# Optimization experiments

Measured on AMD Instinct MI355X. Metric: run time of the kernel, lower is better.

The kernel has to match this reference:

```python
import jax, jax.numpy as jnp
import numpy as np

B, T, V, D, E, A, F = 128, 20, 10000, 1024, 1024, 1024, 2048
ARNET_W = 0.005


def setup_inputs() -> dict:
    key = jax.random.key(0)
    ks = jax.random.split(key, 32)
    p = lambda i, shape: jax.random.normal(ks[i], shape, jnp.float32) * 0.02
    sizes = jax.random.randint(ks[2], (B - 1, 1), 3, T + 1)
    sizes = jnp.concatenate([jnp.array([[T]], dtype=sizes.dtype), sizes], axis=0)  # force max = T
    return dict(
        feats=jax.random.normal(ks[0], (B, 36, F), jnp.float32),
        sequences=jax.random.randint(ks[1], (B, T), 0, V),
        sizes=sizes,
        emb=p(3, (V, E)),
        td_wi=p(4, (4 * D, E + F + D)), td_wh=p(5, (4 * D, D)), td_bi=p(6, (4 * D,)), td_bh=p(7, (4 * D,)),
        lg_wi=p(8, (4 * D, F + D)), lg_wh=p(9, (4 * D, D)), lg_bi=p(10, (4 * D,)), lg_bh=p(11, (4 * D,)),
        ar_wi=p(12, (4 * D, D)), ar_wh=p(13, (4 * D, D)), ar_bi=p(14, (4 * D,)), ar_bh=p(15, (4 * D,)),
        arl_w=p(16, (D, D)), arl_b=p(17, (D,)),
        out_w=p(18, (V, D)), out_b=p(19, (V,)),
        af_w=p(20, (A, F)), af_b=p(21, (A,)),
        ad_w=p(22, (A, D)), ad_b=p(23, (A,)),
        aw_w=p(24, (1, A)), aw_b=p(25, (1,)),
    )


def _lstm(x, h, c, wi, wh, bi, bh):
    # torch.nn.LSTMCell: gates ordered i, f, g, o
    g = x @ wi.T + bi + h @ wh.T + bh
    i, f, gg, o = jnp.split(g, 4, axis=1)
    c2 = jax.nn.sigmoid(f) * c + jax.nn.sigmoid(i) * jnp.tanh(gg)
    return jax.nn.sigmoid(o) * jnp.tanh(c2), c2


def reference(feats, sequences, sizes, emb,
              td_wi, td_wh, td_bi, td_bh,
              lg_wi, lg_wh, lg_bi, lg_bh,
              ar_wi, ar_wh, ar_bi, ar_bh,
              arl_w, arl_b, out_w, out_b,
              af_w, af_b, ad_w, ad_b, aw_w, aw_b):
    # Sort by caption length descending (torch.sort descending)
    order = jnp.argsort(-sizes[:, 0])
    sizes_s = sizes[order, 0]
    feats = feats[order]
    seqs = sequences[order]
    dec_len = sizes_s - 1                      # decode_lengths, max == T-1 by construction
    Tdec = seqs.shape[1] - 1
    featsAvg = feats.mean(axis=1)              # [B, F]
    embs = emb[seqs]                           # [B, T, E]
    # Attention image projection is timestep-invariant: precompute
    img_att = jnp.einsum('brf,af->bra', feats, af_w) + af_b  # [B, 36, A]
    zeros = jnp.zeros((B, D), feats.dtype)

    def step(carry, xs):
        h1, c1, h2, c2, arh, arc, prev_h1, loss = carry
        t, emb_t = xs
        m = (dec_len > t)[:, None].astype(feats.dtype)   # [B,1] active mask (== torch [:bSize] slice)
        bs = m.sum()
        # Top-down LSTM
        nh1, nc1 = _lstm(jnp.concatenate([h2, featsAvg, emb_t], axis=1), h1, c1, td_wi, td_wh, td_bi, td_bh)
        h1 = m * nh1 + (1.0 - m) * h1
        c1 = m * nc1 + (1.0 - m) * c1
        # Visual attention over 36 regions (dropout is identity in eval)
        h1a = h1 @ ad_w.T + ad_b                         # [B, A]
        e = jnp.maximum(h1a[:, None, :] + img_att, 0.0) @ aw_w[0] + aw_b[0]  # [B, 36]
        alpha = jax.nn.softmax(e, axis=1)
        awe = jnp.einsum('br,brf->bf', alpha, feats)     # [B, F]
        # Language LSTM
        nh2, nc2 = _lstm(jnp.concatenate([awe, h1], axis=1), h2, c2, lg_wi, lg_wh, lg_bi, lg_bh)
        h2 = m * nh2 + (1.0 - m) * h2
        c2 = m * nc2 + (1.0 - m) * c2
        # ARNet reconstruction LSTM
        narh, narc = _lstm(h1, arh, arc, ar_wi, ar_wh, ar_bi, ar_bh)
        arh = m * narh + (1.0 - m) * arh
        arc = m * narc + (1.0 - m) * arc
        diff = (arh @ arl_w.T + arl_b) - prev_h1
        lt = jnp.sum(m[:, 0] * jnp.sum(diff * diff, axis=1)) / bs * ARNET_W
        loss = loss + jnp.where(t > 0, lt, jnp.zeros((), feats.dtype))
        pred = m * (h2 @ out_w.T + out_b)                # [B, V], zeros for finished rows
        return (h1, c1, h2, c2, arh, arc, h1, loss), pred

    init = (zeros, zeros, zeros, zeros, zeros, zeros, zeros, jnp.zeros((), feats.dtype))
    xs = (jnp.arange(Tdec), jnp.swapaxes(embs[:, :Tdec], 0, 1))
    (_, _, _, _, _, _, _, loss_ar), preds = jax.lax.scan(step, init, xs)
    preds = jnp.swapaxes(preds, 0, 1)                    # [B, Tdec, V]
    return preds, seqs, order, loss_ar
```

## Files before the change

kernel.cpp:

```cpp
#include <hip/hip_runtime.h>
#include <math.h>

#define B    128
#define T    20
#define TD   19
#define V    10000
#define D    1024
#define E    1024
#define A_DIM 1024
#define F    2048
#define NR   36
#define BD   (B * D)

typedef __attribute__((ext_vector_type(8))) short bf16x8;
typedef __attribute__((ext_vector_type(4))) float f32x4;

__device__ __forceinline__ float sigm(float x) { return 1.f / (1.f + __expf(-x)); }

__device__ __forceinline__ unsigned short f2bf(float f) {
    union { float f; unsigned u; } x; x.f = f;
    unsigned r = x.u + 0x7fffu + ((x.u >> 16) & 1u);
    return (unsigned short)(r >> 16);
}
__device__ __forceinline__ float bf2f(unsigned short u) {
    union { float f; unsigned u; } x; x.u = ((unsigned)u) << 16; return x.f;
}
__device__ __forceinline__ uint4 pack8(const float* __restrict__ src) {
    float4 a = *(const float4*)src, b = *(const float4*)(src + 4);
    union { unsigned short u[8]; uint4 v; } p;
    p.u[0] = f2bf(a.x); p.u[1] = f2bf(a.y); p.u[2] = f2bf(a.z); p.u[3] = f2bf(a.w);
    p.u[4] = f2bf(b.x); p.u[5] = f2bf(b.y); p.u[6] = f2bf(b.z); p.u[7] = f2bf(b.w);
    return p.v;
}

__global__ void k_sort_init(const int* __restrict__ sizes,
                            const int* __restrict__ sequences,
                            int* __restrict__ order,
                            int* __restrict__ active,
                            int* __restrict__ seqs_s,
                            float* __restrict__ out)
{
    int tid = threadIdx.x;
    __shared__ int s_sizes[B];
    __shared__ int s_dl[B];
    s_sizes[tid] = sizes[tid];
    __syncthreads();
    int si = s_sizes[tid];
    int rank = 0;
    for (int j = 0; j < B; ++j) {
        int sj = s_sizes[j];
        if (sj > si || (sj == si && j < tid)) rank++;
    }
    order[rank] = tid;
    __syncthreads();
    int ob = order[tid];
    int dl = s_sizes[ob] - 1;
    s_dl[tid] = dl;
    for (int tt = 0; tt < T; ++tt) {
        int sq = sequences[ob * T + tt];
        seqs_s[tid * T + tt] = sq;
        out[(size_t)B * TD * V + tid * T + tt] = (float)sq;
    }
    out[(size_t)B * TD * V + B * T + tid] = (float)ob;
    __syncthreads();
    if (tid < TD) {
        int c = 0;
        for (int b = 0; b < B; ++b) c += (s_dl[b] > tid) ? 1 : 0;
        active[tid] = c;
    }
    if (tid == 0) out[(size_t)B * TD * V + B * T + B] = 0.f;
}

__global__ void k_zero(float* __restrict__ p, int n) {
    int i = blockIdx.x * 256 + threadIdx.x;
    if (i < n) p[i] = 0.f;
}

__global__ void k_w2bf(const float* __restrict__ s1, int K1,
                       const float* __restrict__ s2, int K2,
                       unsigned short* __restrict__ dst, long total ,
                       int il)
{
    long g = (long)blockIdx.x * 256 + threadIdx.x;
    if (g >= total) return;
    int Kt = K1 + K2;
    int gpr = Kt >> 3;
    int row = (int)(g / gpr);
    int k8 = (int)(g % gpr) << 3;
    if (k8 >= K1 && !s2) {
        uint4 z{};
        *(uint4*)(dst + ((size_t)g << 3)) = z;
        return;
    }
    int srow = il ? ((row & 3) * 1024 + (row >> 2)) : row;
    const float* src = (k8 < K1) ? (s1 + (size_t)srow * K1 + k8)
                                 : (s2 + (size_t)srow * K2 + (k8 - K1));
    *(uint4*)(dst + ((size_t)g << 3)) = pack8(src);
}

__global__ void k_feats2bf(const float* __restrict__ feats, const int* __restrict__ order,
                           unsigned short* __restrict__ dst)
{
    long g = (long)blockIdx.x * 256 + threadIdx.x;
    int row = (int)(g >> 8);
    int k8 = ((int)g & 255) << 3;
    int b = row / NR, r = row - b * NR;
    const float* src = feats + ((size_t)order[b] * NR + r) * F + k8;
    *(uint4*)(dst + (size_t)row * F + k8) = pack8(src);
}

__global__ void k_favg(const float* __restrict__ feats, const int* __restrict__ order,
                       unsigned short* __restrict__ xtd)
{
    int idx = blockIdx.x * 256 + threadIdx.x;
    int b = idx >> 11, f = idx & 2047;
    const float* base = feats + (size_t)order[b] * NR * F + f;
    float s = 0.f;
#pragma unroll
    for (int r = 0; r < NR; ++r) s += base[(size_t)r * F];
    xtd[(size_t)b * 5120 + 1024 + f] = f2bf(s * (1.f / NR));
}

__global__ void k_emb2bf(const float* __restrict__ emb, const int* __restrict__ seqs_s,
                         unsigned short* __restrict__ embs_bf)
{
    long g = (long)blockIdx.x * 256 + threadIdx.x;
    if (g >= (long)B * TD * 128) return;
    int b = (int)(g / (TD * 128));
    int rem = (int)(g - (long)b * (TD * 128));
    int t = rem >> 7, e8 = (rem & 127) << 3;
    const float* src = emb + (size_t)seqs_s[b * T + t] * E + e8;
    *(uint4*)(embs_bf + (((size_t)(b * TD + t)) << 10) + e8) = pack8(src);
}

__global__ void k_embslot(const unsigned short* __restrict__ embs_bf,
                          unsigned short* __restrict__ xtd, int t)
{
    int g = blockIdx.x * 256 + threadIdx.x;
    int b = g >> 7, e8 = (g & 127) << 3;
    *(uint4*)(xtd + (size_t)b * 5120 + 3072 + e8) =
        *(const uint4*)(embs_bf + (((size_t)(b * TD + t)) << 10) + e8);
}

__global__ void k_biasint(const float* __restrict__ bi, const float* __restrict__ bh,
                          const float* __restrict__ extra, float* __restrict__ dst, int n)
{
    int i = blockIdx.x * 256 + threadIdx.x;
    if (i >= n) return;
    if (i < 4096) {
        int j = i >> 2, g = i & 3;
        dst[i] = bi[g * 1024 + j] + bh[g * 1024 + j];
    } else {
        dst[i] = extra[i - 4096];
    }
}

__device__ __forceinline__ void gemm_core(
    const unsigned short* __restrict__ A, int lda,
    const unsigned short* __restrict__ W, int ldw, int Ksub, int N,
    unsigned short* __restrict__ smem,
    int bm, int bn, f32x4 (&acc)[2][2])
{
    int tid = threadIdx.x, l = tid & 63, w = tid >> 6;
    int rsel = l & 15, ksel = (l >> 4) * 8;

    const unsigned short* ap[4];
#pragma unroll
    for (int i = 0; i < 4; ++i) {
        int s = 4 * w + i, mt = s >> 1, subk = s & 1;
        ap[i] = A + (size_t)(bm + mt * 16 + rsel) * lda + subk * 32 + ksel;
    }
    int nt_w = w >> 1, wsub = w & 1;
    int nr = bn + nt_w * 16 + rsel; if (nr >= N) nr = N - 1;
    const unsigned short* wp = W + (size_t)nr * ldw + wsub * 32 + ksel;
    int ntile = Ksub >> 6;

    uint4 rA0_0, rA0_1, rA0_2, rA0_3, rW0;
    uint4 rA1_0, rA1_1, rA1_2, rA1_3, rW1;

    auto load0 = [&]() {
        rA0_0 = *(const uint4*)ap[0]; ap[0] += 64;
        rA0_1 = *(const uint4*)ap[1]; ap[1] += 64;
        rA0_2 = *(const uint4*)ap[2]; ap[2] += 64;
        rA0_3 = *(const uint4*)ap[3]; ap[3] += 64;
        rW0 = *(const uint4*)wp; wp += 64;
    };
    auto load1 = [&]() {
        rA1_0 = *(const uint4*)ap[0]; ap[0] += 64;
        rA1_1 = *(const uint4*)ap[1]; ap[1] += 64;
        rA1_2 = *(const uint4*)ap[2]; ap[2] += 64;
        rA1_3 = *(const uint4*)ap[3]; ap[3] += 64;
        rW1 = *(const uint4*)wp; wp += 64;
    };
    auto stash0 = [&]() {
        unsigned short* As = smem;
        *(uint4*)(As + (4 * w + 0) * 512 + l * 8) = rA0_0;
        *(uint4*)(As + (4 * w + 1) * 512 + l * 8) = rA0_1;
        *(uint4*)(As + (4 * w + 2) * 512 + l * 8) = rA0_2;
        *(uint4*)(As + (4 * w + 3) * 512 + l * 8) = rA0_3;
        *(uint4*)(As + 8192 + w * 512 + l * 8) = rW0;
    };
    auto stash1 = [&]() {
        unsigned short* As = smem + 10240;
        *(uint4*)(As + (4 * w + 0) * 512 + l * 8) = rA1_0;
        *(uint4*)(As + (4 * w + 1) * 512 + l * 8) = rA1_1;
        *(uint4*)(As + (4 * w + 2) * 512 + l * 8) = rA1_2;
        *(uint4*)(As + (4 * w + 3) * 512 + l * 8) = rA1_3;
        *(uint4*)(As + 8192 + w * 512 + l * 8) = rW1;
    };
    auto compute = [&](int p) {
        unsigned short* As = smem + p * 10240;
        unsigned short* Ws = As + 8192;
#pragma unroll
        for (int subk = 0; subk < 2; ++subk) {
            bf16x8 a0 = *(const bf16x8*)(As + (4 * w + subk) * 512 + l * 8);
            bf16x8 a1 = *(const bf16x8*)(As + (4 * w + 2 + subk) * 512 + l * 8);
            bf16x8 b0 = *(const bf16x8*)(Ws + subk * 512 + l * 8);
            bf16x8 b1 = *(const bf16x8*)(Ws + (2 + subk) * 512 + l * 8);
            acc[0][0] = __builtin_amdgcn_mfma_f32_16x16x32_bf16(a0, b0, acc[0][0], 0, 0, 0);
            acc[0][1] = __builtin_amdgcn_mfma_f32_16x16x32_bf16(a0, b1, acc[0][1], 0, 0, 0);
            acc[1][0] = __builtin_amdgcn_mfma_f32_16x16x32_bf16(a1, b0, acc[1][0], 0, 0, 0);
            acc[1][1] = __builtin_amdgcn_mfma_f32_16x16x32_bf16(a1, b1, acc[1][1], 0, 0, 0);
        }
    };

    load0(); load1();
    for (int t = 0; t < ntile; t += 2) {
        stash0();
        if (t + 2 < ntile) load0();
        asm volatile("s_waitcnt lgkmcnt(0)" ::: "memory");
        __builtin_amdgcn_s_barrier();
        compute(0);
        __builtin_amdgcn_s_barrier();
        stash1();
        if (t + 3 < ntile) load1();
        asm volatile("s_waitcnt lgkmcnt(0)" ::: "memory");
        __builtin_amdgcn_s_barrier();
        compute(1);
        __builtin_amdgcn_s_barrier();
    }
}

__global__ __launch_bounds__(256)
void k_gemm(const unsigned short* __restrict__ A, int lda,
            const unsigned short* __restrict__ W, int ldw, int Ksub,
            const float* __restrict__ bias,
            float* __restrict__ C, int ldc, int N,
            int mode, const float* __restrict__ sub, const int* __restrict__ actp,
            float* __restrict__ lossp)
{
    __shared__ __align__(16) unsigned short smem[2 * 10240];
    __shared__ float ps[4];

    int bn = blockIdx.x * 32, bm;
    const unsigned short* Ab = A;
    const unsigned short* Wb = W;
    float* Cb = C;
    if (mode == 4) {
        bm = 0;
        Ab += (size_t)blockIdx.y * Ksub;
        Wb += (size_t)blockIdx.y * Ksub;
        Cb  = C + (size_t)blockIdx.y * 128 * ldc;
    } else {
        bm = blockIdx.y * 128;
    }
    int tid = threadIdx.x, l = tid & 63, w = tid >> 6;

    f32x4 acc[2][2] = {};
    gemm_core(Ab, lda, Wb, ldw, Ksub, N, smem, bm, bn, acc);

    int rg4 = (l >> 4) * 4, cc = l & 15;
    if (mode == 1) {
        int act = actp[blockIdx.y];
        float s = 0.f;
#pragma unroll
        for (int mi = 0; mi < 2; ++mi) {
            int mt = 2 * w + mi;
#pragma unroll
            for (int ni = 0; ni < 2; ++ni) {
                int col = bn + ni * 16 + cc;
                float bb = bias[col];
#pragma unroll
                for (int rg = 0; rg < 4; ++rg) {
                    int row = bm + mt * 16 + rg4 + rg;
                    float v = acc[mi][ni][rg] + bb - sub[(size_t)row * 1024 + col];
                    if ((row & 127) < act) s += v * v;
                }
            }
        }
        for (int o = 32; o > 0; o >>= 1) s += __shfl_down(s, o, 64);
        if (l == 0) ps[w] = s;
        __syncthreads();
        if (tid == 0) {
            float tot = ps[0] + ps[1] + ps[2] + ps[3];
            atomicAdd(lossp, tot * (0.005f / (float)act));
        }
        return;
    }

    if (mode == 3) {
#pragma unroll
        for (int mi = 0; mi < 2; ++mi) {
            int mt = 2 * w + mi;
#pragma unroll
            for (int ni = 0; ni < 2; ++ni) {
                int col = bn + ni * 16 + cc;
                if (col >= N) continue;
                float bb = bias[col];
#pragma unroll
                for (int rg = 0; rg < 4; ++rg) {
                    int row = bm + mt * 16 + rg4 + rg;
                    int tt = row >> 7, b = row & 127;
                    float v = acc[mi][ni][rg] + bb;
                    if (b >= actp[tt]) v = 0.f;
                    C[(size_t)b * ((size_t)TD * V) + (size_t)tt * V + col] = v;
                }
            }
        }
        return;
    }

    if (mode == 4) {
#pragma unroll
        for (int mi = 0; mi < 2; ++mi) {
            int mt = 2 * w + mi;
#pragma unroll
            for (int ni = 0; ni < 2; ++ni) {
                int col = bn + ni * 16 + cc;
#pragma unroll
                for (int rg = 0; rg < 4; ++rg) {
                    int row = mt * 16 + rg4 + rg;
                    Cb[(size_t)row * ldc + col] = acc[mi][ni][rg];
                }
            }
        }
        return;
    }

#pragma unroll
    for (int mi = 0; mi < 2; ++mi) {
        int mt = 2 * w + mi;
#pragma unroll
        for (int ni = 0; ni < 2; ++ni) {
            int col = bn + ni * 16 + cc;
            if (col >= N) continue;
            float bb = bias[col];
#pragma unroll
            for (int rg = 0; rg < 4; ++rg) {
                int row = bm + mt * 16 + rg4 + rg;
                C[(size_t)row * ldc + col] = acc[mi][ni][rg] + bb;
            }
        }
    }
}

__global__ void k_lstm4(const float* __restrict__ p, int ldp, int ns,
                        const float* __restrict__ biasI,
                        float* __restrict__ h, float* __restrict__ c,
                        const int* __restrict__ actp, float* __restrict__ prevh,
                        unsigned short* __restrict__ s1, int ld1,
                        unsigned short* __restrict__ s2, int ld2,
                        unsigned short* __restrict__ s3, int ld3,
                        const unsigned short* __restrict__ embs_bf,
                        unsigned short* __restrict__ xtd_emb, int tnext)
{
    int idx = blockIdx.x * 256 + threadIdx.x;
    if (embs_bf && idx < B * 128) {
        int be = idx >> 7, e8 = (idx & 127) << 3;
        *(uint4*)(xtd_emb + (size_t)be * 5120 + 3072 + e8) =
            *(const uint4*)(embs_bf + (((size_t)(be * TD + tnext)) << 10) + e8);
    }
    int b = idx >> 10;
    if (b >= *actp) return;
    int j = idx & 1023;
    const float* pb = p + (size_t)b * ldp + (j << 2);
    size_t spl = (size_t)128 * ldp;
    float4 g = *(const float4*)pb;
    for (int s = 1; s < ns; ++s) {
        float4 gs = *(const float4*)(pb + (size_t)s * spl);
        g.x += gs.x; g.y += gs.y; g.z += gs.z; g.w += gs.w;
    }
    float4 bb = *(const float4*)(biasI + (j << 2));
    float gi = g.x + bb.x, gf = g.y + bb.y, gg = g.z + bb.z, go = g.w + bb.w;
    size_t ix = (size_t)b * 1024 + j;
    if (prevh) prevh[ix] = h[ix];
    float c2v = sigm(gf) * c[ix] + sigm(gi) * tanhf(gg);
    c[ix] = c2v;
    float hv = sigm(go) * tanhf(c2v);
    h[ix] = hv;
    unsigned short hb = f2bf(hv);
    if (s1) s1[(size_t)b * ld1 + j] = hb;
    if (s2) s2[(size_t)b * ld2 + j] = hb;
    if (s3) s3[(size_t)b * ld3 + j] = hb;
}

__global__ __launch_bounds__(256)
void k_attn_ar(const float* __restrict__ pc, const float* __restrict__ bias_comb,
               const float* __restrict__ img_att,
               const float* __restrict__ aw_w, const float* __restrict__ aw_b,
               const unsigned short* __restrict__ feats_bf,
               unsigned short* __restrict__ xlg,
               float* __restrict__ arh, float* __restrict__ arc,
               const int* __restrict__ actp,
               unsigned short* __restrict__ xar_slot,
               unsigned short* __restrict__ Arout_t)
{
    int b = blockIdx.x;
    int tid = threadIdx.x;
    __shared__ float sh[A_DIM];
    __shared__ float se[NR];
    const float* p0 = pc + (size_t)b * 5120;
    const float* p1 = pc + (size_t)128 * 5120 + (size_t)b * 5120;
    for (int a = tid; a < A_DIM; a += 256)
        sh[a] = p0[4096 + a] + p1[4096 + a] + bias_comb[4096 + a];

    int act = *actp;
    if (b < act) {
#pragma unroll
        for (int u = 0; u < 4; ++u) {
            int j = (tid << 2) + u;
            float4 ga = *(const float4*)(p0 + (j << 2));
            float4 gb = *(const float4*)(p1 + (j << 2));
            float4 bb = *(const float4*)(bias_comb + (j << 2));
            float gi = ga.x + gb.x + bb.x, gf = ga.y + gb.y + bb.y;
            float gg = ga.z + gb.z + bb.z, go = ga.w + gb.w + bb.w;
            size_t ix = (size_t)b * 1024 + j;
            float c2v = sigm(gf) * arc[ix] + sigm(gi) * tanhf(gg);
            arc[ix] = c2v;
            float hv = sigm(go) * tanhf(c2v);
            arh[ix] = hv;
            unsigned short hb = f2bf(hv);
            xar_slot[(size_t)b * 2048 + j] = hb;
            if (Arout_t) Arout_t[(size_t)b * 1024 + j] = hb;
        }
    }
    __syncthreads();

    int wid = tid >> 6, lane = tid & 63;
    for (int r = wid; r < NR; r += 4) {
        const float* row = img_att + ((size_t)b * NR + r) * A_DIM;
        float s = 0.f;
        for (int a = lane; a < A_DIM; a += 64)
            s += fmaxf(sh[a] + row[a], 0.f) * aw_w[a];
        for (int off = 32; off > 0; off >>= 1) s += __shfl_down(s, off, 64);
        if (lane == 0) se[r] = s + aw_b[0];
    }
    __syncthreads();
    if (tid == 0) {
        float m = se[0];
        for (int r = 1; r < NR; ++r) m = fmaxf(m, se[r]);
        float ssum = 0.f;
        for (int r = 0; r < NR; ++r) { float ex = __expf(se[r] - m); se[r] = ex; ssum += ex; }
        float inv = 1.f / ssum;
        for (int r = 0; r < NR; ++r) se[r] *= inv;
    }
    __syncthreads();
    int f8 = tid << 3;
    const unsigned short* fb = feats_bf + (size_t)b * NR * F + f8;
    float s[8] = {};
    for (int r = 0; r < NR; ++r) {
        bf16x8 v = *(const bf16x8*)(fb + (size_t)r * F);
        float a = se[r];
#pragma unroll
        for (int q = 0; q < 8; ++q)
            s[q] += a * bf2f(((const unsigned short*)&v)[q]);
    }
    union { unsigned short u[8]; uint4 v4; } pk;
#pragma unroll
    for (int q = 0; q < 8; ++q) pk.u[q] = f2bf(s[q]);
    *(uint4*)(xlg + (size_t)b * 4096 + f8) = pk.v4;
}

extern "C" void kernel_launch(void* const* d_in, const int* in_sizes, int n_in,
                              void* d_out, int out_size, void* d_ws, size_t ws_size,
                              hipStream_t stream)
{
    const float* feats     = (const float*)d_in[0];
    const int*   sequences = (const int*)d_in[1];
    const int*   sizes     = (const int*)d_in[2];
    const float* emb       = (const float*)d_in[3];
    const float* td_wi = (const float*)d_in[4];
    const float* td_wh = (const float*)d_in[5];
    const float* td_bi = (const float*)d_in[6];
    const float* td_bh = (const float*)d_in[7];
    const float* lg_wi = (const float*)d_in[8];
    const float* lg_wh = (const float*)d_in[9];
    const float* lg_bi = (const float*)d_in[10];
    const float* lg_bh = (const float*)d_in[11];
    const float* ar_wi = (const float*)d_in[12];
    const float* ar_wh = (const float*)d_in[13];
    const float* ar_bi = (const float*)d_in[14];
    const float* ar_bh = (const float*)d_in[15];
    const float* arl_w = (const float*)d_in[16];
    const float* arl_b = (const float*)d_in[17];
    const float* out_w = (const float*)d_in[18];
    const float* out_b = (const float*)d_in[19];
    const float* af_w  = (const float*)d_in[20];
    const float* af_b  = (const float*)d_in[21];
    const float* ad_w  = (const float*)d_in[22];
    const float* ad_b  = (const float*)d_in[23];
    const float* aw_w  = (const float*)d_in[24];
    const float* aw_b  = (const float*)d_in[25];
    float* out = (float*)d_out;

    float* ws = (float*)d_ws;
    size_t off = 0;
    auto alloc = [&](size_t n) { float* p = ws + off; off += n; return p; };
    float* h1   = alloc((size_t)BD);
    float* c1   = alloc((size_t)BD);
    float* h2   = alloc((size_t)BD);
    float* c2   = alloc((size_t)BD);
    float* arh  = alloc((size_t)BD);
    float* arc  = alloc((size_t)BD);
    unsigned short* xtd = (unsigned short*)alloc((size_t)B * 5120 / 2);
    unsigned short* xlg = (unsigned short*)alloc((size_t)B * 4096 / 2);
    unsigned short* xar = (unsigned short*)alloc((size_t)B * 2048 / 2);
    int zero_n = 6 * BD + (B * 5120 + B * 4096 + B * 2048) / 2;
    float* gpart     = alloc((size_t)4 * 128 * 5120);
    float* prevh_all = alloc((size_t)(TD - 1) * BD);
    float* img_att   = alloc((size_t)B * NR * A_DIM);
    float* bias_td   = alloc(4096);
    float* bias_lg   = alloc(4096);
    float* bias_comb = alloc(5120);
    unsigned short* embs_bf  = (unsigned short*)alloc((size_t)B * TD * E / 2);
    unsigned short* feats_bf = (unsigned short*)alloc((size_t)B * NR * F / 2);
    unsigned short* Hout     = (unsigned short*)alloc((size_t)TD * BD / 2);
    unsigned short* Arout    = (unsigned short*)alloc((size_t)(TD - 1) * BD / 2);
    unsigned short* Wtd  = (unsigned short*)alloc((size_t)4096 * 5120 / 2);
    unsigned short* Wlg  = (unsigned short*)alloc((size_t)4096 * 4096 / 2);
    unsigned short* Wcomb = (unsigned short*)alloc((size_t)5120 * 2048 / 2);
    unsigned short* Wout = (unsigned short*)alloc((size_t)10048 * 1024 / 2);
    unsigned short* Warl = (unsigned short*)alloc((size_t)1024 * 1024 / 2);
    unsigned short* Waf  = (unsigned short*)alloc((size_t)1024 * 2048 / 2);
    int* ip     = (int*)(ws + off);
    int* order  = ip; ip += B;
    int* active = ip; ip += TD + 1;
    int* seqs_s = ip; ip += B * T;

    float* loss_ptr = out + (size_t)B * TD * V + B * T + B;

    k_sort_init<<<1, B, 0, stream>>>(sizes, sequences, order, active, seqs_s, out);
    k_zero<<<(zero_n + 255) / 256, 256, 0, stream>>>(h1, zero_n);
    k_favg<<<1024, 256, 0, stream>>>(feats, order, xtd);
    k_emb2bf<<<(B * TD * 128 + 255) / 256, 256, 0, stream>>>(emb, seqs_s, embs_bf);
    k_feats2bf<<<4608, 256, 0, stream>>>(feats, order, feats_bf);
    k_w2bf<<<10240, 256, 0, stream>>>(td_wi, 4096, td_wh, 1024, Wtd, (long)4096 * 640, 1);
    k_w2bf<<<8192, 256, 0, stream>>>(lg_wi, 3072, lg_wh, 1024, Wlg, (long)4096 * 512, 1);
    k_w2bf<<<4096, 256, 0, stream>>>(ar_wi, 1024, ar_wh, 1024, Wcomb, (long)4096 * 256, 1);
    k_w2bf<<<1024, 256, 0, stream>>>(ad_w, 1024, nullptr, 1024,
                                     Wcomb + (size_t)4096 * 2048, (long)1024 * 256, 0);
    k_w2bf<<<5000, 256, 0, stream>>>(out_w, 1024, nullptr, 0, Wout, (long)V * 128, 0);
    k_w2bf<<<512, 256, 0, stream>>>(arl_w, 1024, nullptr, 0, Warl, (long)1024 * 128, 0);
    k_w2bf<<<1024, 256, 0, stream>>>(af_w, 2048, nullptr, 0, Waf, (long)1024 * 256, 0);
    k_biasint<<<16, 256, 0, stream>>>(td_bi, td_bh, nullptr, bias_td, 4096);
    k_biasint<<<16, 256, 0, stream>>>(lg_bi, lg_bh, nullptr, bias_lg, 4096);
    k_biasint<<<20, 256, 0, stream>>>(ar_bi, ar_bh, ad_b, bias_comb, 5120);
    k_gemm<<<dim3(32, 36), 256, 0, stream>>>(
        feats_bf, 2048, Waf, 2048, 2048, af_b,
        img_att, 1024, 1024, 0, nullptr, nullptr, nullptr);
    k_embslot<<<64, 256, 0, stream>>>(embs_bf, xtd, 0);

    for (int t = 0; t < TD; ++t) {
        const int* actp = active + t;
        k_gemm<<<dim3(128, 4), 256, 0, stream>>>(
            xtd, 5120, Wtd, 5120, 1280, nullptr,
            gpart, 4096, 4096, 4, nullptr, nullptr, nullptr);
        k_lstm4<<<512, 256, 0, stream>>>(gpart, 4096, 4, bias_td,
            h1, c1, actp,
            (t > 0) ? prevh_all + (size_t)(t - 1) * BD : nullptr,
            xtd + 4096, 5120, xlg + 2048, 4096, xar, 2048,
            nullptr, nullptr, 0);
        k_gemm<<<dim3(160, 2), 256, 0, stream>>>(
            xar, 2048, Wcomb, 2048, 1024, nullptr,
            gpart, 5120, 5120, 4, nullptr, nullptr, nullptr);
        k_attn_ar<<<B, 256, 0, stream>>>(
            gpart, bias_comb, img_att, aw_w, aw_b, feats_bf, xlg,
            arh, arc, actp, xar + 1024,
            (t > 0) ? Arout + (size_t)(t - 1) * BD : (unsigned short*)nullptr);
        k_gemm<<<dim3(128, 4), 256, 0, stream>>>(
            xlg, 4096, Wlg, 4096, 1024, nullptr,
            gpart, 4096, 4096, 4, nullptr, nullptr, nullptr);
        k_lstm4<<<512, 256, 0, stream>>>(gpart, 4096, 4, bias_lg,
            h2, c2, actp, nullptr,
            xtd, 5120, xlg + 3072, 4096, Hout + (size_t)t * BD, 1024,
            (t + 1 < TD) ? embs_bf : (const unsigned short*)nullptr, xtd, t + 1);
    }

    k_gemm<<<dim3(32, TD - 1), 256, 0, stream>>>(
        Arout, 1024, Warl, 1024, 1024, arl_b,
        nullptr, 0, 1024, 1, prevh_all, active + 1, loss_ptr);
    k_gemm<<<dim3((V + 31) / 32, TD), 256, 0, stream>>>(
        Hout, 1024, Wout, 1024, 1024, out_b,
        out, 0, V, 3, nullptr, active, nullptr);
}
```

Before: 3.227 ms.

## Hoist time-invariant LSTM input projections out of recurrent loop and widen GEMM tiles

Splits the top-down LSTM input GEMM so that the featsAvg projection is computed once and the embedding projection for all timesteps is computed in one batched GEMM before the loop. The per-step GEMM then covers only the h2 and h1 slices, and the LSTM kernel adds the precomputed partials. Split-K is raised to 4 for the AR/attention GEMM, and a templated 64-column tile is used for the image-attention and output GEMMs. Scratch partials are stored in the output buffer before the final logits GEMM overwrites it, which depends on write ordering.

```diff
diff --git a/kernel.cpp b/kernel.cpp
--- a/kernel.cpp
+++ b/kernel.cpp
@@ -133,15 +133,6 @@
     *(uint4*)(embs_bf + (((size_t)(b * TD + t)) << 10) + e8) = pack8(src);
 }
 
-__global__ void k_embslot(const unsigned short* __restrict__ embs_bf,
-                          unsigned short* __restrict__ xtd, int t)
-{
-    int g = blockIdx.x * 256 + threadIdx.x;
-    int b = g >> 7, e8 = (g & 127) << 3;
-    *(uint4*)(xtd + (size_t)b * 5120 + 3072 + e8) =
-        *(const uint4*)(embs_bf + (((size_t)(b * TD + t)) << 10) + e8);
-}
-
 __global__ void k_biasint(const float* __restrict__ bi, const float* __restrict__ bh,
                           const float* __restrict__ extra, float* __restrict__ dst, int n)
 {
@@ -155,12 +146,14 @@
     }
 }
 
+template<int NT>
 __device__ __forceinline__ void gemm_core(
     const unsigned short* __restrict__ A, int lda,
     const unsigned short* __restrict__ W, int ldw, int Ksub, int N,
     unsigned short* __restrict__ smem,
-    int bm, int bn, f32x4 (&acc)[2][2])
-{
+    int bm, int bn, f32x4 (&acc)[2][NT])
+{
+    const int BUF = 8192 + NT * 1024;
     int tid = threadIdx.x, l = tid & 63, w = tid >> 6;
     int rsel = l & 15, ksel = (l >> 4) * 8;
 
@@ -171,26 +164,33 @@
         ap[i] = A + (size_t)(bm + mt * 16 + rsel) * lda + subk * 32 + ksel;
     }
     int nt_w = w >> 1, wsub = w & 1;
-    int nr = bn + nt_w * 16 + rsel; if (nr >= N) nr = N - 1;
-    const unsigned short* wp = W + (size_t)nr * ldw + wsub * 32 + ksel;
+    int nr0 = bn + nt_w * 16 + rsel; if (nr0 >= N) nr0 = N - 1;
+    const unsigned short* wp0 = W + (size_t)nr0 * ldw + wsub * 32 + ksel;
+    const unsigned short* wp1 = wp0;
+    if (NT == 4) {
+        int nr1 = bn + 32 + nt_w * 16 + rsel; if (nr1 >= N) nr1 = N - 1;
+        wp1 = W + (size_t)nr1 * ldw + wsub * 32 + ksel;
+    }
     int ntile = Ksub >> 6;
 
-    uint4 rA0_0, rA0_1, rA0_2, rA0_3, rW0;
-    uint4 rA1_0, rA1_1, rA1_2, rA1_3, rW1;
+    uint4 rA0_0, rA0_1, rA0_2, rA0_3, rW0a, rW0b;
+    uint4 rA1_0, rA1_1, rA1_2, rA1_3, rW1a, rW1b;
 
     auto load0 = [&]() {
         rA0_0 = *(const uint4*)ap[0]; ap[0] += 64;
         rA0_1 = *(const uint4*)ap[1]; ap[1] += 64;
         rA0_2 = *(const uint4*)ap[2]; ap[2] += 64;
         rA0_3 = *(const uint4*)ap[3]; ap[3] += 64;
-        rW0 = *(const uint4*)wp; wp += 64;
+        rW0a = *(const uint4*)wp0; wp0 += 64;
+        if (NT == 4) { rW0b = *(const uint4*)wp1; wp1 += 64; }
     };
     auto load1 = [&]() {
         rA1_0 = *(const uint4*)ap[0]; ap[0] += 64;
         rA1_1 = *(const uint4*)ap[1]; ap[1] += 64;
         rA1_2 = *(const uint4*)ap[2]; ap[2] += 64;
         rA1_3 = *(const uint4*)ap[3]; ap[3] += 64;
-        rW1 = *(const uint4*)wp; wp += 64;
+        rW1a = *(const uint4*)wp0; wp0 += 64;
+        if (NT == 4) { rW1b = *(const uint4*)wp1; wp1 += 64; }
     };
     auto stash0 = [&]() {
         unsigned short* As = smem;
@@ -198,29 +198,31 @@
         *(uint4*)(As + (4 * w + 1) * 512 + l * 8) = rA0_1;
         *(uint4*)(As + (4 * w + 2) * 512 + l * 8) = rA0_2;
         *(uint4*)(As + (4 * w + 3) * 512 + l * 8) = rA0_3;
-        *(uint4*)(As + 8192 + w * 512 + l * 8) = rW0;
+        *(uint4*)(As + 8192 + w * 512 + l * 8) = rW0a;
+        if (NT == 4) *(uint4*)(As + 8192 + (4 + w) * 512 + l * 8) = rW0b;
     };
     auto stash1 = [&]() {
-        unsigned short* As = smem + 10240;
+        unsigned short* As = smem + BUF;
         *(uint4*)(As + (4 * w + 0) * 512 + l * 8) = rA1_0;
         *(uint4*)(As + (4 * w + 1) * 512 + l * 8) = rA1_1;
         *(uint4*)(As + (4 * w + 2) * 512 + l * 8) = rA1_2;
         *(uint4*)(As + (4 * w + 3) * 512 + l * 8) = rA1_3;
-        *(uint4*)(As + 8192 + w * 512 + l * 8) = rW1;
+        *(uint4*)(As + 8192 + w * 512 + l * 8) = rW1a;
+        if (NT == 4) *(uint4*)(As + 8192 + (4 + w) * 512 + l * 8) = rW1b;
     };
     auto compute = [&](int p) {
-        unsigned short* As = smem + p * 10240;
+        unsigned short* As = smem + p * BUF;
         unsigned short* Ws = As + 8192;
 #pragma unroll
         for (int subk = 0; subk < 2; ++subk) {
             bf16x8 a0 = *(const bf16x8*)(As + (4 * w + subk) * 512 + l * 8);
             bf16x8 a1 = *(const bf16x8*)(As + (4 * w + 2 + subk) * 512 + l * 8);
-            bf16x8 b0 = *(const bf16x8*)(Ws + subk * 512 + l * 8);
-            bf16x8 b1 = *(const bf16x8*)(Ws + (2 + subk) * 512 + l * 8);
-            acc[0][0] = __builtin_amdgcn_mfma_f32_16x16x32_bf16(a0, b0, acc[0][0], 0, 0, 0);
-            acc[0][1] = __builtin_amdgcn_mfma_f32_16x16x32_bf16(a0, b1, acc[0][1], 0, 0, 0);
-            acc[1][0] = __builtin_amdgcn_mfma_f32_16x16x32_bf16(a1, b0, acc[1][0], 0, 0, 0);
-            acc[1][1] = __builtin_amdgcn_mfma_f32_16x16x32_bf16(a1, b1, acc[1][1], 0, 0, 0);
+#pragma unroll
+            for (int nt = 0; nt < NT; ++nt) {
+                bf16x8 bb = *(const bf16x8*)(Ws + (nt * 2 + subk) * 512 + l * 8);
+                acc[0][nt] = __builtin_amdgcn_mfma_f32_16x16x32_bf16(a0, bb, acc[0][nt], 0, 0, 0);
+                acc[1][nt] = __builtin_amdgcn_mfma_f32_16x16x32_bf16(a1, bb, acc[1][nt], 0, 0, 0);
+            }
         }
     };
 
@@ -241,6 +243,7 @@
     }
 }
 
+template<int NT>
 __global__ __launch_bounds__(256)
 void k_gemm(const unsigned short* __restrict__ A, int lda,
             const unsigned short* __restrict__ W, int ldw, int Ksub,
@@ -249,25 +252,30 @@
             int mode, const float* __restrict__ sub, const int* __restrict__ actp,
             float* __restrict__ lossp)
 {
-    __shared__ __align__(16) unsigned short smem[2 * 10240];
+    __shared__ __align__(16) unsigned short smem[2 * (8192 + NT * 1024)];
     __shared__ float ps[4];
 
-    int bn = blockIdx.x * 32, bm;
+    int bn = blockIdx.x * (NT * 16), bm;
     const unsigned short* Ab = A;
     const unsigned short* Wb = W;
     float* Cb = C;
-    if (mode == 4) {
+    if (mode == 4 || mode == 6) {
         bm = 0;
-        Ab += (size_t)blockIdx.y * Ksub;
-        Wb += (size_t)blockIdx.y * Ksub;
+        size_t o = (mode == 4) ? (size_t)blockIdx.y * Ksub
+                               : (size_t)(blockIdx.y >> 1) * 4096 + (blockIdx.y & 1) * 512;
+        Ab += o; Wb += o;
         Cb  = C + (size_t)blockIdx.y * 128 * ldc;
     } else {
         bm = blockIdx.y * 128;
     }
     int tid = threadIdx.x, l = tid & 63, w = tid >> 6;
 
-    f32x4 acc[2][2] = {};
-    gemm_core(Ab, lda, Wb, ldw, Ksub, N, smem, bm, bn, acc);
+    f32x4 acc[2][NT];
+#pragma unroll
+    for (int mi = 0; mi < 2; ++mi)
+#pragma unroll
+        for (int ni = 0; ni < NT; ++ni) acc[mi][ni] = (f32x4){0.f, 0.f, 0.f, 0.f};
+    gemm_core<NT>(Ab, lda, Wb, ldw, Ksub, N, smem, bm, bn, acc);
 
     int rg4 = (l >> 4) * 4, cc = l & 15;
     if (mode == 1) {
@@ -277,7 +285,7 @@
         for (int mi = 0; mi < 2; ++mi) {
             int mt = 2 * w + mi;
 #pragma unroll
-            for (int ni = 0; ni < 2; ++ni) {
+            for (int ni = 0; ni < NT; ++ni) {
                 int col = bn + ni * 16 + cc;
                 float bb = bias[col];
 #pragma unroll
@@ -303,7 +311,7 @@
         for (int mi = 0; mi < 2; ++mi) {
             int mt = 2 * w + mi;
 #pragma unroll
-            for (int ni = 0; ni < 2; ++ni) {
+            for (int ni = 0; ni < NT; ++ni) {
                 int col = bn + ni * 16 + cc;
                 if (col >= N) continue;
                 float bb = bias[col];
@@ -320,12 +328,12 @@
         return;
     }
 
-    if (mode == 4) {
+    if (mode == 4 || mode == 6) {
 #pragma unroll
         for (int mi = 0; mi < 2; ++mi) {
             int mt = 2 * w + mi;
 #pragma unroll
-            for (int ni = 0; ni < 2; ++ni) {
+            for (int ni = 0; ni < NT; ++ni) {
                 int col = bn + ni * 16 + cc;
 #pragma unroll
                 for (int rg = 0; rg < 4; ++rg) {
@@ -341,10 +349,10 @@
     for (int mi = 0; mi < 2; ++mi) {
         int mt = 2 * w + mi;
 #pragma unroll
-        for (int ni = 0; ni < 2; ++ni) {
+        for (int ni = 0; ni < NT; ++ni) {
             int col = bn + ni * 16 + cc;
             if (col >= N) continue;
-            float bb = bias[col];
+            float bb = bias ? bias[col] : 0.f;
 #pragma unroll
             for (int rg = 0; rg < 4; ++rg) {
                 int row = bm + mt * 16 + rg4 + rg;
@@ -356,20 +364,15 @@
 
 __global__ void k_lstm4(const float* __restrict__ p, int ldp, int ns,
                         const float* __restrict__ biasI,
+                        const float* __restrict__ e1,
+                        const float* __restrict__ e2, int e2ldb,
                         float* __restrict__ h, float* __restrict__ c,
                         const int* __restrict__ actp, float* __restrict__ prevh,
                         unsigned short* __restrict__ s1, int ld1,
                         unsigned short* __restrict__ s2, int ld2,
-                        unsigned short* __restrict__ s3, int ld3,
-                        const unsigned short* __restrict__ embs_bf,
-                        unsigned short* __restrict__ xtd_emb, int tnext)
+                        unsigned short* __restrict__ s3, int ld3)
 {
     int idx = blockIdx.x * 256 + threadIdx.x;
-    if (embs_bf && idx < B * 128) {
-        int be = idx >> 7, e8 = (idx & 127) << 3;
-        *(uint4*)(xtd_emb + (size_t)be * 5120 + 3072 + e8) =
-            *(const uint4*)(embs_bf + (((size_t)(be * TD + tnext)) << 10) + e8);
-    }
     int b = idx >> 10;
     if (b >= *actp) return;
     int j = idx & 1023;
@@ -379,6 +382,14 @@
     for (int s = 1; s < ns; ++s) {
         float4 gs = *(const float4*)(pb + (size_t)s * spl);
         g.x += gs.x; g.y += gs.y; g.z += gs.z; g.w += gs.w;
+    }
+    if (e1) {
+        float4 ge = *(const float4*)(e1 + ((size_t)b << 12) + (j << 2));
+        g.x += ge.x; g.y += ge.y; g.z += ge.z; g.w += ge.w;
+    }
+    if (e2) {
+        float4 ge = *(const float4*)(e2 + (size_t)b * e2ldb + (j << 2));
+        g.x += ge.x; g.y += ge.y; g.z += ge.z; g.w += ge.w;
     }
     float4 bb = *(const float4*)(biasI + (j << 2));
     float gi = g.x + bb.x, gf = g.y + bb.y, gg = g.z + bb.z, go = g.w + bb.w;
@@ -409,21 +420,29 @@
     int tid = threadIdx.x;
     __shared__ float sh[A_DIM];
     __shared__ float se[NR];
-    const float* p0 = pc + (size_t)b * 5120;
-    const float* p1 = pc + (size_t)128 * 5120 + (size_t)b * 5120;
-    for (int a = tid; a < A_DIM; a += 256)
-        sh[a] = p0[4096 + a] + p1[4096 + a] + bias_comb[4096 + a];
+    const float* pb = pc + (size_t)b * 5120;
+    const size_t spl = (size_t)128 * 5120;
+    for (int a = tid; a < A_DIM; a += 256) {
+        float v = bias_comb[4096 + a];
+#pragma unroll
+        for (int s = 0; s < 4; ++s) v += pb[s * spl + 4096 + a];
+        sh[a] = v;
+    }
 
     int act = *actp;
     if (b < act) {
 #pragma unroll
         for (int u = 0; u < 4; ++u) {
             int j = (tid << 2) + u;
-            float4 ga = *(const float4*)(p0 + (j << 2));
-            float4 gb = *(const float4*)(p1 + (j << 2));
+            float4 g = *(const float4*)(pb + (j << 2));
+#pragma unroll
+            for (int s = 1; s < 4; ++s) {
+                float4 gs = *(const float4*)(pb + s * spl + (j << 2));
+                g.x += gs.x; g.y += gs.y; g.z += gs.z; g.w += gs.w;
+            }
             float4 bb = *(const float4*)(bias_comb + (j << 2));
-            float gi = ga.x + gb.x + bb.x, gf = ga.y + gb.y + bb.y;
-            float gg = ga.z + gb.z + bb.z, go = ga.w + gb.w + bb.w;
+            float gi = g.x + bb.x, gf = g.y + bb.y;
+            float gg = g.z + bb.z, go = g.w + bb.w;
             size_t ix = (size_t)b * 1024 + j;
             float c2v = sigm(gf) * arc[ix] + sigm(gi) * tanhf(gg);
             arc[ix] = c2v;
@@ -503,6 +522,9 @@
     const float* aw_b  = (const float*)d_in[25];
     float* out = (float*)d_out;
 
+    float* gemb  = out;
+    float* gpart = out + (size_t)B * TD * 4096;
+
     float* ws = (float*)d_ws;
     size_t off = 0;
     auto alloc = [&](size_t n) { float* p = ws + off; off += n; return p; };
@@ -516,7 +538,7 @@
     unsigned short* xlg = (unsigned short*)alloc((size_t)B * 4096 / 2);
     unsigned short* xar = (unsigned short*)alloc((size_t)B * 2048 / 2);
     int zero_n = 6 * BD + (B * 5120 + B * 4096 + B * 2048) / 2;
-    float* gpart     = alloc((size_t)4 * 128 * 5120);
+    float* gfa       = alloc((size_t)B * 4096);
     float* prevh_all = alloc((size_t)(TD - 1) * BD);
     float* img_att   = alloc((size_t)B * NR * A_DIM);
     float* bias_td   = alloc(4096);
@@ -529,7 +551,7 @@
     unsigned short* Wtd  = (unsigned short*)alloc((size_t)4096 * 5120 / 2);
     unsigned short* Wlg  = (unsigned short*)alloc((size_t)4096 * 4096 / 2);
     unsigned short* Wcomb = (unsigned short*)alloc((size_t)5120 * 2048 / 2);
-    unsigned short* Wout = (unsigned short*)alloc((size_t)10048 * 1024 / 2);
+    unsigned short* Wout = (unsigned short*)alloc((size_t)V * 1024 / 2);
     unsigned short* Warl = (unsigned short*)alloc((size_t)1024 * 1024 / 2);
     unsigned short* Waf  = (unsigned short*)alloc((size_t)1024 * 2048 / 2);
     int* ip     = (int*)(ws + off);
@@ -555,41 +577,46 @@
     k_biasint<<<16, 256, 0, stream>>>(td_bi, td_bh, nullptr, bias_td, 4096);
     k_biasint<<<16, 256, 0, stream>>>(lg_bi, lg_bh, nullptr, bias_lg, 4096);
     k_biasint<<<20, 256, 0, stream>>>(ar_bi, ar_bh, ad_b, bias_comb, 5120);
-    k_gemm<<<dim3(32, 36), 256, 0, stream>>>(
+    k_gemm<4><<<dim3(16, 36), 256, 0, stream>>>(
         feats_bf, 2048, Waf, 2048, 2048, af_b,
         img_att, 1024, 1024, 0, nullptr, nullptr, nullptr);
-    k_embslot<<<64, 256, 0, stream>>>(embs_bf, xtd, 0);
+    k_gemm<2><<<dim3(128, 1), 256, 0, stream>>>(
+        xtd + 1024, 5120, Wtd + 1024, 5120, 2048, nullptr,
+        gfa, 4096, 4096, 0, nullptr, nullptr, nullptr);
+    k_gemm<2><<<dim3(128, TD), 256, 0, stream>>>(
+        embs_bf, 1024, Wtd + 3072, 5120, 1024, nullptr,
+        gemb, 4096, 4096, 0, nullptr, nullptr, nullptr);
 
     for (int t = 0; t < TD; ++t) {
         const int* actp = active + t;
-        k_gemm<<<dim3(128, 4), 256, 0, stream>>>(
-            xtd, 5120, Wtd, 5120, 1280, nullptr,
-            gpart, 4096, 4096, 4, nullptr, nullptr, nullptr);
+        k_gemm<2><<<dim3(128, 4), 256, 0, stream>>>(
+            xtd, 5120, Wtd, 5120, 512, nullptr,
+            gpart, 4096, 4096, 6, nullptr, nullptr, nullptr);
         k_lstm4<<<512, 256, 0, stream>>>(gpart, 4096, 4, bias_td,
+            gfa, gemb + (size_t)t * 4096, TD * 4096,
             h1, c1, actp,
             (t > 0) ? prevh_all + (size_t)(t - 1) * BD : nullptr,
-            xtd + 4096, 5120, xlg + 2048, 4096, xar, 2048,
-            nullptr, nullptr, 0);
-        k_gemm<<<dim3(160, 2), 256, 0, stream>>>(
-            xar, 2048, Wcomb, 2048, 1024, nullptr,
+            xtd + 4096, 5120, xlg + 2048, 4096, xar, 2048);
+        k_gemm<2><<<dim3(160, 4), 256, 0, stream>>>(
+            xar, 2048, Wcomb, 2048, 512, nullptr,
             gpart, 5120, 5120, 4, nullptr, nullptr, nullptr);
         k_attn_ar<<<B, 256, 0, stream>>>(
             gpart, bias_comb, img_att, aw_w, aw_b, feats_bf, xlg,
             arh, arc, actp, xar + 1024,
             (t > 0) ? Arout + (size_t)(t - 1) * BD : (unsigned short*)nullptr);
-        k_gemm<<<dim3(128, 4), 256, 0, stream>>>(
+        k_gemm<2><<<dim3(128, 4), 256, 0, stream>>>(
             xlg, 4096, Wlg, 4096, 1024, nullptr,
             gpart, 4096, 4096, 4, nullptr, nullptr, nullptr);
         k_lstm4<<<512, 256, 0, stream>>>(gpart, 4096, 4, bias_lg,
+            nullptr, nullptr, 0,
             h2, c2, actp, nullptr,
-            xtd, 5120, xlg + 3072, 4096, Hout + (size_t)t * BD, 1024,
-            (t + 1 < TD) ? embs_bf : (const unsigned short*)nullptr, xtd, t + 1);
-    }
-
-    k_gemm<<<dim3(32, TD - 1), 256, 0, stream>>>(
+            xtd, 5120, xlg + 3072, 4096, Hout + (size_t)t * BD, 1024);
+    }
+
+    k_gemm<2><<<dim3(32, TD - 1), 256, 0, stream>>>(
         Arout, 1024, Warl, 1024, 1024, arl_b,
         nullptr, 0, 1024, 1, prevh_all, active + 1, loss_ptr);
-    k_gemm<<<dim3((V + 31) / 32, TD), 256, 0, stream>>>(
+    k_gemm<4><<<dim3((V + 63) / 64, TD), 256, 0, stream>>>(
         Hout, 1024, Wout, 1024, 1024, out_b,
         out, 0, V, 3, nullptr, active, nullptr);
 }
```

Result: faster. 2.946 ms (-8.7%).
